# Performance work log

Measured on AMD Instinct MI355X. Metric: run time of the kernel, lower is better.

The kernel has to match this reference:

```python
import jax, jax.numpy as jnp
import numpy as np

NUM_SIN = 8
HIDDEN = 64
COND = 128
OUT = 4
SQRT2 = 1.4142135623730951


def coords_to_sinusoidals(coords):
    # coords: [..., 2]; per-frequency blocks of 4: [sin_x, sin_y, cos_x, cos_y]
    freqs = 2.0 ** jnp.arange(NUM_SIN, dtype=coords.dtype)  # mult freq_type, multiplier=2
    ang = coords[..., None, :] * freqs[:, None]              # [..., 8, 2]
    emb = jnp.concatenate([jnp.sin(ang), jnp.cos(ang)], axis=-1)  # [..., 8, 4]
    return emb.reshape(coords.shape[:-1] + (2 * 2 * NUM_SIN,))


def equal_linear(x, w, b, lrelu):
    scale = 1.0 / np.sqrt(w.shape[1])  # lr_mul = 1
    y = x @ (w * scale).T + b
    if lrelu:
        y = jax.nn.leaky_relu(y, 0.2) * SQRT2  # fused_lrelu
    return y


def setup_inputs() -> dict:
    key = jax.random.key(0)
    ks = jax.random.split(key, 8)
    coords = jax.random.normal(ks[0], (8, 256, 256, 2), dtype=jnp.float32)
    c = jax.random.normal(ks[1], (8, COND), dtype=jnp.float32)
    freq_unlock = jax.random.uniform(ks[2], (1,), dtype=jnp.float32)
    in1 = 2 * 2 * NUM_SIN + COND  # 160
    in2 = HIDDEN + COND           # 192
    w1 = jax.random.normal(ks[3], (HIDDEN, in1), dtype=jnp.float32)
    w2 = jax.random.normal(ks[4], (HIDDEN, in2), dtype=jnp.float32)
    w3 = jax.random.normal(ks[5], (HIDDEN, in2), dtype=jnp.float32)
    w4 = jax.random.normal(ks[6], (OUT, in2), dtype=jnp.float32)
    b1 = jnp.zeros((HIDDEN,), jnp.float32)
    b2 = jnp.zeros((HIDDEN,), jnp.float32)
    b3 = jnp.zeros((HIDDEN,), jnp.float32)
    b4 = jnp.zeros((OUT,), jnp.float32)
    return {"coords": coords, "c": c, "freq_unlock": freq_unlock,
            "w1": w1, "b1": b1, "w2": w2, "b2": b2,
            "w3": w3, "b3": b3, "w4": w4, "b4": b4}


def reference(coords, c, freq_unlock, w1, b1, w2, b2, w3, b3, w4, b4):
    B, H, W, _ = coords.shape
    emb = coords_to_sinusoidals(coords / 10.0)  # [B,H,W,32]
    # progressive frequency masking
    limits = jnp.arange(1, NUM_SIN + 1, dtype=coords.dtype) / (NUM_SIN + 1)
    weights = jnp.clip((freq_unlock[0] - limits) * (NUM_SIN + 1), 0.0, 1.0)  # [8]
    emb = emb * jnp.repeat(weights, 4)  # blocks of 4 per frequency
    x = emb.reshape(B * H * W, -1)
    cf = jnp.broadcast_to(c[:, None, None, :], (B, H, W, COND)).reshape(B * H * W, COND)
    h = equal_linear(jnp.concatenate([x, cf], -1), w1, b1, True)
    h = equal_linear(jnp.concatenate([h, cf], -1), w2, b2, True)
    h = equal_linear(jnp.concatenate([h, cf], -1), w3, b3, True)
    h = equal_linear(jnp.concatenate([h, cf], -1), w4, b4, False)
    out = h.reshape(B, H, W, OUT)
    # radius masking
    radius = jnp.sqrt(jnp.sum(coords ** 2, axis=-1, keepdims=True))
    out = out * (1.0 - jnp.tanh(jax.nn.relu(radius - 1.0)))
    return out
```

## Files before the change

### kernel.cpp

```cpp
#include <hip/hip_runtime.h>
#include <math.h>


typedef _Float16 half2v __attribute__((ext_vector_type(2)));
typedef __fp16   fp16x2 __attribute__((ext_vector_type(2)));
typedef _Float16 half4v __attribute__((ext_vector_type(4)));
typedef _Float16 half8  __attribute__((ext_vector_type(8)));
typedef float f32x16 __attribute__((ext_vector_type(16)));

#define SCALE1 0.0790569415042094833f
#define SCALE2 0.0721687836487032206f
#define SQRT2F 1.41421356237309515f

#define FE_L1 0
#define FE_L2 256
#define FE_L3 768
#define FE_L4 1280
#define OFF_CB1 6144
#define OFF_CB2 6656
#define OFF_CB3 7168
#define OFF_CB4 7680

__global__ __launch_bounds__(256) void prep_kernel(
    const float* __restrict__ c, const float* __restrict__ fu,
    const float* __restrict__ w1, const float* __restrict__ b1,
    const float* __restrict__ w2, const float* __restrict__ b2,
    const float* __restrict__ w3, const float* __restrict__ b3,
    const float* __restrict__ w4, const float* __restrict__ b4,
    float* __restrict__ ws)
{
  int t = blockIdx.x * 256 + threadIdx.x;
  if (t < 12288) {
    _Float16* fr = (_Float16*)ws;
    int e, Ktm;
    const float* w; float scale; int stride; bool perm;
    if (t < 2048)       { e = t;         Ktm = 2; w = w1; scale = SCALE1;          stride = 160; perm = false; }
    else if (t < 6144)  { e = t - 2048;  Ktm = 4; w = w2; scale = SCALE2 * SQRT2F; stride = 192; perm = true;  }
    else if (t < 10240) { e = t - 6144;  Ktm = 4; w = w3; scale = SCALE2 * SQRT2F; stride = 192; perm = true;  }
    else                { e = t - 10240; Ktm = 4; w = w4; scale = SCALE2 * SQRT2F; stride = 192; perm = true;  }
    int til  = e >> 9;
    int lane = (e >> 3) & 63;
    int r    = e & 7;
    int q    = lane >> 5;
    int mt = til / Ktm, kt = til - mt * Ktm;
    int j = 32 * mt + (lane & 31);
    int k;
    if (perm) {
      k = 32 * (kt >> 1) + 16 * (kt & 1) + 8 * (r >> 2) + 4 * q + (r & 3);
    } else {
      k = 16 * kt + 8 * q + r;
    }
    float val;
    if (t < 2048) {
      float mw = (fu[0] - (float)((k >> 2) + 1) * (1.0f / 9.0f)) * 9.0f;
      mw = fminf(fmaxf(mw, 0.0f), 1.0f);
      val = w[j * stride + k] * scale * mw;
    } else if (t >= 10240) {
      val = (j < 4) ? w[j * stride + k] * scale : 0.0f;
    } else {
      val = w[j * stride + k] * scale;
    }
    fr[t] = (_Float16)val;
  } else if (t < 12288 + 2048) {
    int u = t - 12288;
    int grp = u >> 9;
    const float* wr; float bias; float scale; int outoff;
    int b, j;
    if (grp < 3) {
      b = (u & 511) >> 6; j = u & 63;
      if (grp == 0)      { wr = w1 + j * 160 + 32; bias = b1[j]; scale = SCALE1; outoff = OFF_CB1 + b * 64 + j; }
      else if (grp == 1) { wr = w2 + j * 192 + 64; bias = b2[j]; scale = SCALE2; outoff = OFF_CB2 + b * 64 + j; }
      else               { wr = w3 + j * 192 + 64; bias = b3[j]; scale = SCALE2; outoff = OFF_CB3 + b * 64 + j; }
    } else {
      int u2 = u - 1536;
      if (u2 >= 32) return;
      b = u2 >> 2; j = u2 & 3;
      wr = w4 + j * 192 + 64; bias = b4[j]; scale = SCALE2; outoff = OFF_CB4 + b * 4 + j;
    }
    const float4* wv = (const float4*)wr;
    const float4* cv = (const float4*)(c + b * 128);
    float4 s = make_float4(0.f, 0.f, 0.f, 0.f);
    #pragma unroll
    for (int k = 0; k < 32; ++k) {
      float4 a = wv[k], d = cv[k];
      s.x = fmaf(a.x, d.x, s.x);
      s.y = fmaf(a.y, d.y, s.y);
      s.z = fmaf(a.z, d.z, s.z);
      s.w = fmaf(a.w, d.w, s.w);
    }
    float dot = (s.x + s.y) + (s.z + s.w);
    ws[outoff] = fmaf(scale, dot, bias);
  }
}

__global__ __launch_bounds__(256, 4) void decoder_main(
    const float2* __restrict__ coords, const float* __restrict__ ws,
    float4* __restrict__ out)
{
  const int lane = threadIdx.x & 63;
  const int wave = threadIdx.x >> 6;
  const int base = blockIdx.x * 256 + wave * 64;
  const int b    = base >> 16;
  const int col  = lane & 31;
  const bool hi  = lane >= 32;
  const int q4   = hi ? 4 : 0;

  const half8* __restrict__ frags = (const half8*)ws;
  const float* __restrict__ cb1 = ws + OFF_CB1 + b * 64;
  const float* __restrict__ cb2 = ws + OFF_CB2 + b * 64;
  const float* __restrict__ cb3 = ws + OFF_CB3 + b * 64;
  const float* __restrict__ cb4 = ws + OFF_CB4 + b * 4;

  const int p0 = base + col, p1 = base + 32 + col;
  const float2 cc0 = coords[p0];
  const float2 cc1 = coords[p1];

  half8 bf[2][2];
  {
    const float qm = hi ? 0.4f : 0.1f;
    const float xs0 = cc0.x * qm, ys0 = cc0.y * qm;
    const float xs1 = cc1.x * qm, ys1 = cc1.y * qm;
    #pragma unroll
    for (int kt = 0; kt < 2; ++kt) {
      #pragma unroll
      for (int r = 0; r < 8; ++r) {
        const float mul = (float)(1 << (4 * kt + (r >> 2)));
        float a0, a1;
        if      ((r & 3) == 0) { a0 = __sinf(xs0 * mul); a1 = __sinf(xs1 * mul); }
        else if ((r & 3) == 1) { a0 = __sinf(ys0 * mul); a1 = __sinf(ys1 * mul); }
        else if ((r & 3) == 2) { a0 = __cosf(xs0 * mul); a1 = __cosf(xs1 * mul); }
        else                   { a0 = __cosf(ys0 * mul); a1 = __cosf(ys1 * mul); }
        bf[0][kt][r] = (_Float16)a0;
        bf[1][kt][r] = (_Float16)a1;
      }
    }
  }

  f32x16 acc[2][2];
  half8 nbf[2][4];

  auto lrelu = [](float v) { return fmaxf(v, 0.2f * v); };

  auto transition = [&]() {
    #pragma unroll
    for (int mt = 0; mt < 2; ++mt)
      #pragma unroll
      for (int nt = 0; nt < 2; ++nt) {
        #pragma unroll
        for (int h = 0; h < 2; ++h) {
          half2v pp[4];
          #pragma unroll
          for (int p = 0; p < 4; ++p) {
            fp16x2 t = __builtin_amdgcn_cvt_pkrtz(
                lrelu(acc[mt][nt][8 * h + 2 * p]),
                lrelu(acc[mt][nt][8 * h + 2 * p + 1]));
            pp[p] = __builtin_bit_cast(half2v, t);
          }
          half4v q0 = __builtin_shufflevector(pp[0], pp[1], 0, 1, 2, 3);
          half4v q1 = __builtin_shufflevector(pp[2], pp[3], 0, 1, 2, 3);
          nbf[nt][2 * mt + h] = __builtin_shufflevector(q0, q1, 0, 1, 2, 3, 4, 5, 6, 7);
        }
      }
  };

  auto init_acc = [&](const float* __restrict__ cb) {
    #pragma unroll
    for (int mt = 0; mt < 2; ++mt)
      #pragma unroll
      for (int g = 0; g < 4; ++g) {
        const float4 f = *(const float4*)(cb + 32 * mt + 8 * g + q4);
        acc[mt][0][4 * g + 0] = f.x; acc[mt][1][4 * g + 0] = f.x;
        acc[mt][0][4 * g + 1] = f.y; acc[mt][1][4 * g + 1] = f.y;
        acc[mt][0][4 * g + 2] = f.z; acc[mt][1][4 * g + 2] = f.z;
        acc[mt][0][4 * g + 3] = f.w; acc[mt][1][4 * g + 3] = f.w;
      }
  };

  init_acc(cb1);
  #pragma unroll
  for (int kt = 0; kt < 2; ++kt) {
    half8 a0 = frags[FE_L1 + (0 * 2 + kt) * 64 + lane];
    half8 a1 = frags[FE_L1 + (1 * 2 + kt) * 64 + lane];
    acc[0][0] = __builtin_amdgcn_mfma_f32_32x32x16_f16(a0, bf[0][kt], acc[0][0], 0, 0, 0);
    acc[0][1] = __builtin_amdgcn_mfma_f32_32x32x16_f16(a0, bf[1][kt], acc[0][1], 0, 0, 0);
    acc[1][0] = __builtin_amdgcn_mfma_f32_32x32x16_f16(a1, bf[0][kt], acc[1][0], 0, 0, 0);
    acc[1][1] = __builtin_amdgcn_mfma_f32_32x32x16_f16(a1, bf[1][kt], acc[1][1], 0, 0, 0);
  }
  transition();

  #pragma unroll
  for (int layer = 0; layer < 2; ++layer) {
    const int fe = layer == 0 ? FE_L2 : FE_L3;
    init_acc(layer == 0 ? cb2 : cb3);
    #pragma unroll
    for (int kt = 0; kt < 4; ++kt) {
      half8 a0 = frags[fe + (0 * 4 + kt) * 64 + lane];
      half8 a1 = frags[fe + (1 * 4 + kt) * 64 + lane];
      acc[0][0] = __builtin_amdgcn_mfma_f32_32x32x16_f16(a0, nbf[0][kt], acc[0][0], 0, 0, 0);
      acc[0][1] = __builtin_amdgcn_mfma_f32_32x32x16_f16(a0, nbf[1][kt], acc[0][1], 0, 0, 0);
      acc[1][0] = __builtin_amdgcn_mfma_f32_32x32x16_f16(a1, nbf[0][kt], acc[1][0], 0, 0, 0);
      acc[1][1] = __builtin_amdgcn_mfma_f32_32x32x16_f16(a1, nbf[1][kt], acc[1][1], 0, 0, 0);
    }
    transition();
  }

  f32x16 acc4[2];
  {
    const float4 f = *(const float4*)cb4;
    #pragma unroll
    for (int r = 0; r < 16; ++r) {
      float bv = (!hi && r < 4) ? ((const float*)&f)[r] : 0.0f;
      acc4[0][r] = bv; acc4[1][r] = bv;
    }
  }
  #pragma unroll
  for (int kt = 0; kt < 4; ++kt) {
    half8 a0 = frags[FE_L4 + kt * 64 + lane];
    acc4[0] = __builtin_amdgcn_mfma_f32_32x32x16_f16(a0, nbf[0][kt], acc4[0], 0, 0, 0);
    acc4[1] = __builtin_amdgcn_mfma_f32_32x32x16_f16(a0, nbf[1][kt], acc4[1], 0, 0, 0);
  }

  if (!hi) {
    #pragma unroll
    for (int nt = 0; nt < 2; ++nt) {
      const float2 cc = nt ? cc1 : cc0;
      const float rad = sqrtf(cc.x * cc.x + cc.y * cc.y);
      const float tt = fmaxf(rad - 1.0f, 0.0f);
      const float m = 2.0f / (__expf(2.0f * tt) + 1.0f);
      out[nt ? p1 : p0] = make_float4(acc4[nt][0] * m, acc4[nt][1] * m,
                                      acc4[nt][2] * m, acc4[nt][3] * m);
    }
  }
}

extern "C" void kernel_launch(void* const* d_in, const int* in_sizes, int n_in,
                              void* d_out, int out_size, void* d_ws, size_t ws_size,
                              hipStream_t stream) {
  const float* coords = (const float*)d_in[0];
  const float* c      = (const float*)d_in[1];
  const float* fu     = (const float*)d_in[2];
  const float* w1     = (const float*)d_in[3];
  const float* b1     = (const float*)d_in[4];
  const float* w2     = (const float*)d_in[5];
  const float* b2     = (const float*)d_in[6];
  const float* w3     = (const float*)d_in[7];
  const float* b3     = (const float*)d_in[8];
  const float* w4     = (const float*)d_in[9];
  const float* b4     = (const float*)d_in[10];
  float* ws  = (float*)d_ws;
  float* out = (float*)d_out;

  int npix = in_sizes[0] / 2;

  prep_kernel<<<56, 256, 0, stream>>>(c, fu, w1, b1, w2, b2, w3, b3, w4, b4, ws);
  decoder_main<<<npix / 256, 256, 0, stream>>>(
      (const float2*)coords, ws, (float4*)out);
}
```

Measured before the change: 97.44 us.

## Fuse weight prep into decoder kernel, staging fragments and cond biases in LDS

Removes the separate prep kernel. Each block of the main kernel now packs the fp16 MFMA weight fragments and computes the per-batch condition bias dot products itself, then stores both in shared memory and reads them from there. This saves one kernel launch and the workspace round trip through global memory. In exchange, every one of the 2048 blocks redoes the packing and the 196 dot products of length 128, adds a __syncthreads, and uses about 25KB of LDS, which could reduce occupancy.

```diff
diff --git a/kernel.cpp b/kernel.cpp
--- a/kernel.cpp
+++ b/kernel.cpp
@@ -16,100 +16,99 @@
 #define FE_L2 256
 #define FE_L3 768
 #define FE_L4 1280
-#define OFF_CB1 6144
-#define OFF_CB2 6656
-#define OFF_CB3 7168
-#define OFF_CB4 7680
-
-__global__ __launch_bounds__(256) void prep_kernel(
+#define FE_TOT 1536
+
+__global__ __launch_bounds__(256, 4) void decoder_fused(
+    const float2* __restrict__ coords,
     const float* __restrict__ c, const float* __restrict__ fu,
     const float* __restrict__ w1, const float* __restrict__ b1,
     const float* __restrict__ w2, const float* __restrict__ b2,
     const float* __restrict__ w3, const float* __restrict__ b3,
     const float* __restrict__ w4, const float* __restrict__ b4,
-    float* __restrict__ ws)
+    float4* __restrict__ out)
 {
-  int t = blockIdx.x * 256 + threadIdx.x;
-  if (t < 12288) {
-    _Float16* fr = (_Float16*)ws;
-    int e, Ktm;
-    const float* w; float scale; int stride; bool perm;
-    if (t < 2048)       { e = t;         Ktm = 2; w = w1; scale = SCALE1;          stride = 160; perm = false; }
-    else if (t < 6144)  { e = t - 2048;  Ktm = 4; w = w2; scale = SCALE2 * SQRT2F; stride = 192; perm = true;  }
-    else if (t < 10240) { e = t - 6144;  Ktm = 4; w = w3; scale = SCALE2 * SQRT2F; stride = 192; perm = true;  }
-    else                { e = t - 10240; Ktm = 4; w = w4; scale = SCALE2 * SQRT2F; stride = 192; perm = true;  }
-    int til  = e >> 9;
-    int lane = (e >> 3) & 63;
-    int r    = e & 7;
-    int q    = lane >> 5;
-    int mt = til / Ktm, kt = til - mt * Ktm;
-    int j = 32 * mt + (lane & 31);
-    int k;
-    if (perm) {
-      k = 32 * (kt >> 1) + 16 * (kt & 1) + 8 * (r >> 2) + 4 * q + (r & 3);
+  __shared__ __align__(16) _Float16 sfr_raw[FE_TOT * 8];
+  __shared__ __align__(16) float scb[196];
+  half8* __restrict__ sfr = (half8*)sfr_raw;
+
+  const int tid  = threadIdx.x;
+  const int bpx  = blockIdx.x * 256;
+  const int b    = bpx >> 16;
+
+  const float freq_unlock = fu[0];
+  auto pack = [&](int idx, const float* __restrict__ w, float scale,
+                  int stride, bool perm, bool isL1, bool isL4, int Ktm,
+                  int ebase) {
+    const int til = idx >> 6, le = idx & 63, q = le >> 5;
+    const int mt = til / Ktm, kt = til - mt * Ktm;
+    const int j = 32 * mt + (le & 31);
+    const int kbase = perm ? (32 * (kt >> 1) + 16 * (kt & 1) + 4 * q)
+                           : (16 * kt + 8 * q);
+    half8 v;
+    if (isL4 && j >= 4) {
+      #pragma unroll
+      for (int r = 0; r < 8; ++r) v[r] = (_Float16)0.0f;
     } else {
-      k = 16 * kt + 8 * q + r;
-    }
-    float val;
-    if (t < 2048) {
-      float mw = (fu[0] - (float)((k >> 2) + 1) * (1.0f / 9.0f)) * 9.0f;
-      mw = fminf(fmaxf(mw, 0.0f), 1.0f);
-      val = w[j * stride + k] * scale * mw;
-    } else if (t >= 10240) {
-      val = (j < 4) ? w[j * stride + k] * scale : 0.0f;
+      const float4 lo = *(const float4*)(w + j * stride + kbase);
+      const float4 up = *(const float4*)(w + j * stride + kbase + (perm ? 8 : 4));
+      float vals[8] = {lo.x, lo.y, lo.z, lo.w, up.x, up.y, up.z, up.w};
+      #pragma unroll
+      for (int r = 0; r < 8; ++r) {
+        float s = scale;
+        if (isL1) {
+          const int k = kbase + r;
+          float mw = (freq_unlock - (float)((k >> 2) + 1) * (1.0f / 9.0f)) * 9.0f;
+          s *= fminf(fmaxf(mw, 0.0f), 1.0f);
+        }
+        v[r] = (_Float16)(vals[r] * s);
+      }
+    }
+    sfr[ebase + idx] = v;
+  };
+  pack(tid,       w1, SCALE1,          160, false, true,  false, 2, FE_L1);
+  pack(tid,       w2, SCALE2 * SQRT2F, 192, true,  false, false, 4, FE_L2);
+  pack(tid + 256, w2, SCALE2 * SQRT2F, 192, true,  false, false, 4, FE_L2);
+  pack(tid,       w3, SCALE2 * SQRT2F, 192, true,  false, false, 4, FE_L3);
+  pack(tid + 256, w3, SCALE2 * SQRT2F, 192, true,  false, false, 4, FE_L3);
+  pack(tid,       w4, SCALE2 * SQRT2F, 192, true,  false, true,  4, FE_L4);
+
+  if (tid < 196) {
+    const float* wr; float bias, scl;
+    if (tid < 192) {
+      const int grp = tid >> 6, j = tid & 63;
+      if (grp == 0)      { wr = w1 + j * 160 + 32; bias = b1[j]; scl = SCALE1; }
+      else if (grp == 1) { wr = w2 + j * 192 + 64; bias = b2[j]; scl = SCALE2; }
+      else               { wr = w3 + j * 192 + 64; bias = b3[j]; scl = SCALE2; }
     } else {
-      val = w[j * stride + k] * scale;
-    }
-    fr[t] = (_Float16)val;
-  } else if (t < 12288 + 2048) {
-    int u = t - 12288;
-    int grp = u >> 9;
-    const float* wr; float bias; float scale; int outoff;
-    int b, j;
-    if (grp < 3) {
-      b = (u & 511) >> 6; j = u & 63;
-      if (grp == 0)      { wr = w1 + j * 160 + 32; bias = b1[j]; scale = SCALE1; outoff = OFF_CB1 + b * 64 + j; }
-      else if (grp == 1) { wr = w2 + j * 192 + 64; bias = b2[j]; scale = SCALE2; outoff = OFF_CB2 + b * 64 + j; }
-      else               { wr = w3 + j * 192 + 64; bias = b3[j]; scale = SCALE2; outoff = OFF_CB3 + b * 64 + j; }
-    } else {
-      int u2 = u - 1536;
-      if (u2 >= 32) return;
-      b = u2 >> 2; j = u2 & 3;
-      wr = w4 + j * 192 + 64; bias = b4[j]; scale = SCALE2; outoff = OFF_CB4 + b * 4 + j;
+      const int j = tid - 192;
+      wr = w4 + j * 192 + 64; bias = b4[j]; scl = SCALE2;
     }
     const float4* wv = (const float4*)wr;
     const float4* cv = (const float4*)(c + b * 128);
-    float4 s = make_float4(0.f, 0.f, 0.f, 0.f);
+    float4 s4 = make_float4(0.f, 0.f, 0.f, 0.f);
     #pragma unroll
     for (int k = 0; k < 32; ++k) {
-      float4 a = wv[k], d = cv[k];
-      s.x = fmaf(a.x, d.x, s.x);
-      s.y = fmaf(a.y, d.y, s.y);
-      s.z = fmaf(a.z, d.z, s.z);
-      s.w = fmaf(a.w, d.w, s.w);
-    }
-    float dot = (s.x + s.y) + (s.z + s.w);
-    ws[outoff] = fmaf(scale, dot, bias);
-  }
-}
-
-__global__ __launch_bounds__(256, 4) void decoder_main(
-    const float2* __restrict__ coords, const float* __restrict__ ws,
-    float4* __restrict__ out)
-{
-  const int lane = threadIdx.x & 63;
-  const int wave = threadIdx.x >> 6;
-  const int base = blockIdx.x * 256 + wave * 64;
-  const int b    = base >> 16;
+      const float4 a = wv[k], d = cv[k];
+      s4.x = fmaf(a.x, d.x, s4.x);
+      s4.y = fmaf(a.y, d.y, s4.y);
+      s4.z = fmaf(a.z, d.z, s4.z);
+      s4.w = fmaf(a.w, d.w, s4.w);
+    }
+    scb[tid] = fmaf(scl, (s4.x + s4.y) + (s4.z + s4.w), bias);
+  }
+  __syncthreads();
+
+  const int lane = tid & 63;
+  const int wave = tid >> 6;
+  const int base = bpx + wave * 64;
   const int col  = lane & 31;
   const bool hi  = lane >= 32;
   const int q4   = hi ? 4 : 0;
 
-  const half8* __restrict__ frags = (const half8*)ws;
-  const float* __restrict__ cb1 = ws + OFF_CB1 + b * 64;
-  const float* __restrict__ cb2 = ws + OFF_CB2 + b * 64;
-  const float* __restrict__ cb3 = ws + OFF_CB3 + b * 64;
-  const float* __restrict__ cb4 = ws + OFF_CB4 + b * 4;
+  const float* __restrict__ cb1 = scb;
+  const float* __restrict__ cb2 = scb + 64;
+  const float* __restrict__ cb3 = scb + 128;
+  const float* __restrict__ cb4 = scb + 192;
 
   const int p0 = base + col, p1 = base + 32 + col;
   const float2 cc0 = coords[p0];
@@ -179,8 +178,8 @@
   init_acc(cb1);
   #pragma unroll
   for (int kt = 0; kt < 2; ++kt) {
-    half8 a0 = frags[FE_L1 + (0 * 2 + kt) * 64 + lane];
-    half8 a1 = frags[FE_L1 + (1 * 2 + kt) * 64 + lane];
+    half8 a0 = sfr[FE_L1 + (0 * 2 + kt) * 64 + lane];
+    half8 a1 = sfr[FE_L1 + (1 * 2 + kt) * 64 + lane];
     acc[0][0] = __builtin_amdgcn_mfma_f32_32x32x16_f16(a0, bf[0][kt], acc[0][0], 0, 0, 0);
     acc[0][1] = __builtin_amdgcn_mfma_f32_32x32x16_f16(a0, bf[1][kt], acc[0][1], 0, 0, 0);
     acc[1][0] = __builtin_amdgcn_mfma_f32_32x32x16_f16(a1, bf[0][kt], acc[1][0], 0, 0, 0);
@@ -194,8 +193,8 @@
     init_acc(layer == 0 ? cb2 : cb3);
     #pragma unroll
     for (int kt = 0; kt < 4; ++kt) {
-      half8 a0 = frags[fe + (0 * 4 + kt) * 64 + lane];
-      half8 a1 = frags[fe + (1 * 4 + kt) * 64 + lane];
+      half8 a0 = sfr[fe + (0 * 4 + kt) * 64 + lane];
+      half8 a1 = sfr[fe + (1 * 4 + kt) * 64 + lane];
       acc[0][0] = __builtin_amdgcn_mfma_f32_32x32x16_f16(a0, nbf[0][kt], acc[0][0], 0, 0, 0);
       acc[0][1] = __builtin_amdgcn_mfma_f32_32x32x16_f16(a0, nbf[1][kt], acc[0][1], 0, 0, 0);
       acc[1][0] = __builtin_amdgcn_mfma_f32_32x32x16_f16(a1, nbf[0][kt], acc[1][0], 0, 0, 0);
@@ -206,16 +205,17 @@
 
   f32x16 acc4[2];
   {
-    const float4 f = *(const float4*)cb4;
-    #pragma unroll
-    for (int r = 0; r < 16; ++r) {
-      float bv = (!hi && r < 4) ? ((const float*)&f)[r] : 0.0f;
-      acc4[0][r] = bv; acc4[1][r] = bv;
+    const float c0 = cb4[0], c1 = cb4[1], c2 = cb4[2], c3 = cb4[3];
+    #pragma unroll
+    for (int r = 0; r < 16; ++r) { acc4[0][r] = 0.f; acc4[1][r] = 0.f; }
+    if (!hi) {
+      acc4[0][0] = c0; acc4[0][1] = c1; acc4[0][2] = c2; acc4[0][3] = c3;
+      acc4[1][0] = c0; acc4[1][1] = c1; acc4[1][2] = c2; acc4[1][3] = c3;
     }
   }
   #pragma unroll
   for (int kt = 0; kt < 4; ++kt) {
-    half8 a0 = frags[FE_L4 + kt * 64 + lane];
+    half8 a0 = sfr[FE_L4 + kt * 64 + lane];
     acc4[0] = __builtin_amdgcn_mfma_f32_32x32x16_f16(a0, nbf[0][kt], acc4[0], 0, 0, 0);
     acc4[1] = __builtin_amdgcn_mfma_f32_32x32x16_f16(a0, nbf[1][kt], acc4[1], 0, 0, 0);
   }
@@ -247,12 +247,11 @@
   const float* b3     = (const float*)d_in[8];
   const float* w4     = (const float*)d_in[9];
   const float* b4     = (const float*)d_in[10];
-  float* ws  = (float*)d_ws;
   float* out = (float*)d_out;
 
   int npix = in_sizes[0] / 2;
 
-  prep_kernel<<<56, 256, 0, stream>>>(c, fu, w1, b1, w2, b2, w3, b3, w4, b4, ws);
-  decoder_main<<<npix / 256, 256, 0, stream>>>(
-      (const float2*)coords, ws, (float4*)out);
+  decoder_fused<<<npix / 256, 256, 0, stream>>>(
+      (const float2*)coords, c, fu, w1, b1, w2, b2, w3, b3, w4, b4,
+      (float4*)out);
 }
```

Result: slower. 113.4 us (+16.4%).
